# Kernel optimization log

Hardware: AMD Instinct MI355X
Metric: run time of the kernel (lower is better)

The kernel has to match this reference:

```python
import jax, jax.numpy as jnp
import numpy as np
import math

N_NODES = 100000
N_EDGES = 3200000
F_IN = 512
HID = 128
N_CLS = 16


def setup_inputs() -> dict:
    key = jax.random.key(0)
    k = jax.random.split(key, 6)
    x = jax.random.normal(k[0], (N_NODES, F_IN), dtype=jnp.float32)
    edge_index = jax.random.randint(k[1], (2, N_EDGES), 0, N_NODES, dtype=jnp.int32)
    W1 = jax.random.normal(k[2], (F_IN, HID), dtype=jnp.float32) / np.sqrt(F_IN)
    W2 = jax.random.normal(k[3], (HID, HID), dtype=jnp.float32) / np.sqrt(HID)
    W3 = jax.random.normal(k[4], (N_CLS, HID), dtype=jnp.float32) / np.sqrt(HID)
    b3 = jnp.zeros((N_CLS,), dtype=jnp.float32)
    return {"x": x, "edge_index": edge_index, "W1": W1, "W2": W2, "W3": W3, "b3": b3}


def _sym_norm(edge_index, num_nodes, dtype):
    # add self loops with fill_value = trunc(log2(average_node_degree))
    E = edge_index.shape[1]
    fill = float(math.trunc(math.log2(E / num_nodes)))
    loops = jnp.arange(num_nodes, dtype=edge_index.dtype)
    row = jnp.concatenate([edge_index[0], loops])
    col = jnp.concatenate([edge_index[1], loops])
    w = jnp.concatenate([jnp.ones((E,), dtype), jnp.full((num_nodes,), fill, dtype)])
    deg = jax.ops.segment_sum(w, row, num_segments=num_nodes)
    deg_inv_sqrt = jnp.where(deg > 0, jax.lax.rsqrt(deg), 0.0)
    norm = deg_inv_sqrt[row] * w * deg_inv_sqrt[col]
    return row, col, norm


def reference(x, edge_index, W1, W2, W3, b3):
    N = x.shape[0]
    row, col, norm = _sym_norm(edge_index, N, x.dtype)

    def gcn(h, W):
        h = h @ W                                   # [N, d_out]
        msg = norm[:, None] * h[col]                # gather + scale, [E', d_out]
        return jax.ops.segment_sum(msg, row, num_segments=N)

    h = jax.nn.relu(gcn(x, W1))      # layer 1 + srelu (threshold clamped at 0)
    h = gcn(h, W2)                   # layer 2
    # dropout p=0.5 is identity in eval mode
    return h @ W3.T + b3             # linear classifier [N, n_classes]
```

## Files before the change

kernel.cpp:

```cpp
#include <hip/hip_runtime.h>
#include <cmath>

typedef __attribute__((ext_vector_type(8))) short short8;
typedef __attribute__((ext_vector_type(8))) unsigned short ushort8;
typedef __attribute__((ext_vector_type(4))) float f32x4;
typedef __attribute__((ext_vector_type(2))) float f32x2;
typedef __attribute__((ext_vector_type(4))) unsigned int uint4v;
typedef __attribute__((ext_vector_type(2))) int int2v;

#define EPB 4096
#define BCAP 20480

__device__ inline float bf16_lo(unsigned int p) {
  union { unsigned int i; float f; } v; v.i = p << 16; return v.f;
}
__device__ inline float bf16_hi(unsigned int p) {
  union { unsigned int i; float f; } v; v.i = p & 0xffff0000u; return v.f;
}
__device__ inline f32x2 bf2(unsigned int p) {
  union { unsigned int i; float f; } lo, hi;
  lo.i = p << 16;
  hi.i = p & 0xffff0000u;
  return (f32x2){lo.f, hi.f};
}
__device__ inline float bf16u(unsigned short w) {
  union { unsigned int i; float f; } v; v.i = (unsigned int)w << 16; return v.f;
}
__device__ inline unsigned short f32_to_bf16(float f) {
  union { float f; unsigned int i; } v; v.f = f;
  unsigned int x = v.i;
  x += 0x7fffu + ((x >> 16) & 1u);
  return (unsigned short)(x >> 16);
}
__device__ inline unsigned int cvt_pk_bf16(float a, float b) {
  unsigned int r;
  asm("v_cvt_pk_bf16_f32 %0, %1, %2" : "=v"(r) : "v"(a), "v"(b));
  return r;
}
__device__ inline f32x2 pk_add(f32x2 a, f32x2 b) {
  f32x2 d;
  asm("v_pk_add_f32 %0, %1, %2" : "=v"(d) : "v"(a), "v"(b));
  return d;
}

__global__ __launch_bounds__(256) void bin_k(const int* __restrict__ rows,
                                             const int* __restrict__ cols,
                                             int* __restrict__ bucket_cursor,
                                             unsigned int* __restrict__ binned, int E) {
  __shared__ int lhist[256];
  __shared__ int gbase[256];
  __shared__ int loff[256];
  const int t = threadIdx.x;
  const int base = blockIdx.x * EPB;
  lhist[t] = 0;
  __syncthreads();

  int bk[16];
  unsigned int pk[16];
#pragma unroll
  for (int j = 0; j < 16; ++j) {
    int e = base + j * 256 + t;
    if (e < E) {
      int r = rows[e];
      int c = cols[e];
      bk[j] = r >> 9;
      pk[j] = ((unsigned int)(r & 511) << 17) | (unsigned int)c;
      atomicAdd(&lhist[bk[j]], 1);
    } else {
      bk[j] = -1;
    }
  }
  __syncthreads();
  if (lhist[t] > 0) gbase[t] = atomicAdd(&bucket_cursor[t], lhist[t]);
  loff[t] = 0;
  __syncthreads();
#pragma unroll
  for (int j = 0; j < 16; ++j) {
    if (bk[j] >= 0) {
      int rank = gbase[bk[j]] + atomicAdd(&loff[bk[j]], 1);
      if (rank < BCAP) binned[(size_t)bk[j] * BCAP + rank] = pk[j];
    }
  }
}

__global__ __launch_bounds__(1024) void sort_k(const unsigned int* __restrict__ binned,
                                               const int* __restrict__ bucket_cursor,
                                               int2v* __restrict__ rowse,
                                               float* __restrict__ dis,
                                               int* __restrict__ col_sorted,
                                               int* __restrict__ perm,
                                               int N, float fill) {
  __shared__ int sorted[BCAP];
  __shared__ int cnt[512];
  __shared__ int cur[512];
  __shared__ int dh[512];
  __shared__ int wsum[8];
  const int b = blockIdx.x;
  const int t = threadIdx.x;
  const int start = b * BCAP;
  const int rbase = b << 9;
  int c = bucket_cursor[b];
  if (c > BCAP) c = BCAP;

  auto scan512 = [&](int v) -> int {
    int x = v;
#pragma unroll
    for (int d = 1; d < 64; d <<= 1) {
      int u = __shfl_up(x, d, 64);
      if ((t & 63) >= d) x += u;
    }
    if (t < 512 && (t & 63) == 63) wsum[t >> 6] = x;
    __syncthreads();
    if (t < 64) {
      int s = (t < 8) ? wsum[t] : 0;
#pragma unroll
      for (int d = 1; d < 8; d <<= 1) {
        int u = __shfl_up(s, d, 64);
        if (t >= d) s += u;
      }
      if (t < 8) wsum[t] = s;
    }
    __syncthreads();
    int off = (t >= 64 && t < 512) ? wsum[(t >> 6) - 1] : 0;
    return x + off;
  };

  unsigned int ent[20];
#pragma unroll
  for (int j = 0; j < 20; ++j) {
    int i = j * 1024 + t;
    ent[j] = (i < c) ? binned[start + i] : 0xFFFFFFFFu;
  }

  if (t < 512) cnt[t] = 0;
  __syncthreads();
#pragma unroll
  for (int j = 0; j < 20; ++j)
    if (ent[j] != 0xFFFFFFFFu) atomicAdd(&cnt[ent[j] >> 17], 1);
  __syncthreads();

  int v = (t < 512) ? cnt[t] : 0;
  int incl = scan512(v);
  int excl = incl - v;
  if (t < 512) {
    cur[t] = excl;
    int r = rbase + t;
    if (r < N) {
      rowse[r] = (int2v){start + excl, start + excl + v};
      float d = (float)v + fill;
      dis[r] = d > 0.f ? rsqrtf(d) : 0.f;
    }
  }
  __syncthreads();

#pragma unroll
  for (int j = 0; j < 20; ++j) {
    if (ent[j] != 0xFFFFFFFFu) {
      int rl = (int)(ent[j] >> 17);
      int pos = atomicAdd(&cur[rl], 1);
      sorted[pos] = (int)(ent[j] & 0x1FFFFu);
    }
  }
  __syncthreads();

  for (int i = t; i < c; i += 1024)
    col_sorted[start + i] = sorted[i];

  if (t < 512) dh[t] = 0;
  __syncthreads();
  int key = 0;
  if (t < 512) {
    key = 511 - (v < 511 ? v : 511);
    atomicAdd(&dh[key], 1);
  }
  __syncthreads();
  int hv = (t < 512) ? dh[t] : 0;
  int hincl = scan512(hv);
  if (t < 512) dh[t] = hincl - hv;
  __syncthreads();
  if (t < 512) {
    int rank = atomicAdd(&dh[key], 1);
    perm[rbase + rank] = rbase + t;
  }
}

__global__ __launch_bounds__(256) void cast_w_k(const float* __restrict__ W1,
                                                const float* __restrict__ W2,
                                                const float* __restrict__ W3,
                                                unsigned short* __restrict__ W1t,
                                                unsigned short* __restrict__ W2t,
                                                unsigned short* __restrict__ W3b,
                                                int FIN) {
  int g = blockIdx.x * 256 + threadIdx.x;
  int n1 = FIN * 128;
  if (g < n1) {
    int n = g & 127, k = g >> 7;
    W1t[n * FIN + k] = f32_to_bf16(W1[(size_t)k * 128 + n]);
  } else if (g < n1 + 128 * 128) {
    int gg = g - n1;
    int n = gg & 127, k = gg >> 7;
    W2t[n * 128 + k] = f32_to_bf16(W2[k * 128 + n]);
  } else if (g < n1 + 128 * 128 + 16 * 128) {
    int gg = g - n1 - 128 * 128;
    W3b[gg] = f32_to_bf16(W3[gg]);
  }
}

__global__ __launch_bounds__(256) void gemm_k(const void* __restrict__ Aq, int a_is_f32,
                                              int M, int K,
                                              const unsigned short* __restrict__ Bt,
                                              const float* __restrict__ dis,
                                              unsigned short* __restrict__ C) {
  __shared__ unsigned short Al[128 * 40];
  __shared__ unsigned short Bl[128 * 40];
  const int t = threadIdx.x;
  const int bm = blockIdx.x * 128;
  const int lane = t & 63;
  const int wave = t >> 6;
  const int wm = (wave >> 1) * 64;
  const int wn = (wave & 1) * 64;
  const int l15 = lane & 15;
  const int l4 = lane >> 4;

  f32x4 acc[4][4];
#pragma unroll
  for (int a = 0; a < 4; ++a)
#pragma unroll
    for (int b = 0; b < 4; ++b) acc[a][b] = (f32x4){0.f, 0.f, 0.f, 0.f};

  const int am = t >> 1;
  const int ak = (t & 1) * 16;
  const int bn = t >> 1;
  const int bk = (t & 1) * 16;
  const int arow = bm + am;
  const bool arow_ok = arow < M;

  auto load_a = [&](int k0, ushort8& o0, ushort8& o1) {
    o0 = (ushort8){0, 0, 0, 0, 0, 0, 0, 0};
    o1 = (ushort8){0, 0, 0, 0, 0, 0, 0, 0};
    if (arow_ok) {
      if (a_is_f32) {
        const float* p = (const float*)Aq + (size_t)arow * K + k0 + ak;
        f32x4 f0 = *(const f32x4*)(p);
        f32x4 f1 = *(const f32x4*)(p + 4);
        f32x4 f2 = *(const f32x4*)(p + 8);
        f32x4 f3 = *(const f32x4*)(p + 12);
        union { unsigned int u[4]; ushort8 v8; } c0, c1;
        c0.u[0] = cvt_pk_bf16(f0[0], f0[1]);
        c0.u[1] = cvt_pk_bf16(f0[2], f0[3]);
        c0.u[2] = cvt_pk_bf16(f1[0], f1[1]);
        c0.u[3] = cvt_pk_bf16(f1[2], f1[3]);
        c1.u[0] = cvt_pk_bf16(f2[0], f2[1]);
        c1.u[1] = cvt_pk_bf16(f2[2], f2[3]);
        c1.u[2] = cvt_pk_bf16(f3[0], f3[1]);
        c1.u[3] = cvt_pk_bf16(f3[2], f3[3]);
        o0 = c0.v8;
        o1 = c1.v8;
      } else {
        const unsigned short* p = (const unsigned short*)Aq + (size_t)arow * K + k0 + ak;
        o0 = *(const ushort8*)p;
        o1 = *(const ushort8*)(p + 8);
      }
    }
  };

  ushort8 av0, av1;
  load_a(0, av0, av1);
  ushort8 bv0 = *(const ushort8*)(Bt + (size_t)bn * K + bk);
  ushort8 bv1 = *(const ushort8*)(Bt + (size_t)bn * K + bk + 8);

  for (int k0 = 0; k0 < K; k0 += 32) {
    *(ushort8*)&Al[am * 40 + ak] = av0;
    *(ushort8*)&Al[am * 40 + ak + 8] = av1;
    *(ushort8*)&Bl[bn * 40 + bk] = bv0;
    *(ushort8*)&Bl[bn * 40 + bk + 8] = bv1;
    __syncthreads();

    const int kn = k0 + 32;
    if (kn < K) {
      load_a(kn, av0, av1);
      bv0 = *(const ushort8*)(Bt + (size_t)bn * K + kn + bk);
      bv1 = *(const ushort8*)(Bt + (size_t)bn * K + kn + bk + 8);
    }

    short8 af[4];
#pragma unroll
    for (int mt = 0; mt < 4; ++mt)
      af[mt] = *(const short8*)&Al[(wm + mt * 16 + l15) * 40 + l4 * 8];
#pragma unroll
    for (int nt = 0; nt < 4; ++nt) {
      short8 bfr = *(const short8*)&Bl[(wn + nt * 16 + l15) * 40 + l4 * 8];
#pragma unroll
      for (int mt = 0; mt < 4; ++mt)
        acc[mt][nt] = __builtin_amdgcn_mfma_f32_16x16x32_bf16(af[mt], bfr, acc[mt][nt], 0, 0, 0);
    }
    __syncthreads();
  }

#pragma unroll
  for (int mt = 0; mt < 4; ++mt) {
    int rbase = bm + wm + mt * 16 + l4 * 4;
#pragma unroll
    for (int r = 0; r < 4; ++r) {
      int row = rbase + r;
      if (row < M) {
        float dr = dis[row];
#pragma unroll
        for (int nt = 0; nt < 4; ++nt) {
          int col = wn + nt * 16 + l15;
          C[(size_t)row * 128 + col] = f32_to_bf16(acc[mt][nt][r] * dr);
        }
      }
    }
  }
}

__global__ __launch_bounds__(256) void agg_k(const unsigned short* __restrict__ hs,
                                             const int2v* __restrict__ rowse,
                                             const int* __restrict__ cols,
                                             const float* __restrict__ dis,
                                             const int* __restrict__ perm,
                                             unsigned short* __restrict__ out_bf,
                                             const unsigned short* __restrict__ W3b,
                                             const float* __restrict__ b3,
                                             float* __restrict__ fcout,
                                             int N, float fill, int mode) {
  const int q = blockIdx.x * 16 + (threadIdx.x >> 4);
  const unsigned int fl = threadIdx.x & 15;
  const int rid = perm[q];
  if (rid >= N) return;
  const char* __restrict__ hsc = (const char*)hs;
  const unsigned int flo = fl << 4;

  int2v se = rowse[rid];
  int e = se.x;
  const int end = se.y;

  f32x2 a0 = {0.f, 0.f}, a1 = {0.f, 0.f}, a2 = {0.f, 0.f}, a3 = {0.f, 0.f};

  for (; e + 8 <= end; e += 8) {
    unsigned int c0 = (unsigned int)cols[e];
    unsigned int c1 = (unsigned int)cols[e + 1];
    unsigned int c2 = (unsigned int)cols[e + 2];
    unsigned int c3 = (unsigned int)cols[e + 3];
    unsigned int c4 = (unsigned int)cols[e + 4];
    unsigned int c5 = (unsigned int)cols[e + 5];
    unsigned int c6 = (unsigned int)cols[e + 6];
    unsigned int c7 = (unsigned int)cols[e + 7];
    uint4v p0 = *(const uint4v*)(hsc + ((c0 << 8) | flo));
    uint4v p1 = *(const uint4v*)(hsc + ((c1 << 8) | flo));
    uint4v p2 = *(const uint4v*)(hsc + ((c2 << 8) | flo));
    uint4v p3 = *(const uint4v*)(hsc + ((c3 << 8) | flo));
    uint4v p4 = *(const uint4v*)(hsc + ((c4 << 8) | flo));
    uint4v p5 = *(const uint4v*)(hsc + ((c5 << 8) | flo));
    uint4v p6 = *(const uint4v*)(hsc + ((c6 << 8) | flo));
    uint4v p7 = *(const uint4v*)(hsc + ((c7 << 8) | flo));
    a0 = pk_add(a0, bf2(p0[0])); a1 = pk_add(a1, bf2(p0[1]));
    a2 = pk_add(a2, bf2(p0[2])); a3 = pk_add(a3, bf2(p0[3]));
    a0 = pk_add(a0, bf2(p1[0])); a1 = pk_add(a1, bf2(p1[1]));
    a2 = pk_add(a2, bf2(p1[2])); a3 = pk_add(a3, bf2(p1[3]));
    a0 = pk_add(a0, bf2(p2[0])); a1 = pk_add(a1, bf2(p2[1]));
    a2 = pk_add(a2, bf2(p2[2])); a3 = pk_add(a3, bf2(p2[3]));
    a0 = pk_add(a0, bf2(p3[0])); a1 = pk_add(a1, bf2(p3[1]));
    a2 = pk_add(a2, bf2(p3[2])); a3 = pk_add(a3, bf2(p3[3]));
    a0 = pk_add(a0, bf2(p4[0])); a1 = pk_add(a1, bf2(p4[1]));
    a2 = pk_add(a2, bf2(p4[2])); a3 = pk_add(a3, bf2(p4[3]));
    a0 = pk_add(a0, bf2(p5[0])); a1 = pk_add(a1, bf2(p5[1]));
    a2 = pk_add(a2, bf2(p5[2])); a3 = pk_add(a3, bf2(p5[3]));
    a0 = pk_add(a0, bf2(p6[0])); a1 = pk_add(a1, bf2(p6[1]));
    a2 = pk_add(a2, bf2(p6[2])); a3 = pk_add(a3, bf2(p6[3]));
    a0 = pk_add(a0, bf2(p7[0])); a1 = pk_add(a1, bf2(p7[1]));
    a2 = pk_add(a2, bf2(p7[2])); a3 = pk_add(a3, bf2(p7[3]));
  }
  for (; e + 4 <= end; e += 4) {
    unsigned int c0 = (unsigned int)cols[e];
    unsigned int c1 = (unsigned int)cols[e + 1];
    unsigned int c2 = (unsigned int)cols[e + 2];
    unsigned int c3 = (unsigned int)cols[e + 3];
    uint4v p0 = *(const uint4v*)(hsc + ((c0 << 8) | flo));
    uint4v p1 = *(const uint4v*)(hsc + ((c1 << 8) | flo));
    uint4v p2 = *(const uint4v*)(hsc + ((c2 << 8) | flo));
    uint4v p3 = *(const uint4v*)(hsc + ((c3 << 8) | flo));
    a0 = pk_add(a0, bf2(p0[0])); a1 = pk_add(a1, bf2(p0[1]));
    a2 = pk_add(a2, bf2(p0[2])); a3 = pk_add(a3, bf2(p0[3]));
    a0 = pk_add(a0, bf2(p1[0])); a1 = pk_add(a1, bf2(p1[1]));
    a2 = pk_add(a2, bf2(p1[2])); a3 = pk_add(a3, bf2(p1[3]));
    a0 = pk_add(a0, bf2(p2[0])); a1 = pk_add(a1, bf2(p2[1]));
    a2 = pk_add(a2, bf2(p2[2])); a3 = pk_add(a3, bf2(p2[3]));
    a0 = pk_add(a0, bf2(p3[0])); a1 = pk_add(a1, bf2(p3[1]));
    a2 = pk_add(a2, bf2(p3[2])); a3 = pk_add(a3, bf2(p3[3]));
  }
  for (; e < end; ++e) {
    unsigned int c = (unsigned int)cols[e];
    uint4v p = *(const uint4v*)(hsc + ((c << 8) | flo));
    a0 = pk_add(a0, bf2(p[0])); a1 = pk_add(a1, bf2(p[1]));
    a2 = pk_add(a2, bf2(p[2])); a3 = pk_add(a3, bf2(p[3]));
  }

  uint4v ps = *(const uint4v*)(hsc + (((unsigned int)rid << 8) | flo));
  float dr = dis[rid];
  float v[8];
  v[0] = dr * (a0.x + fill * bf16_lo(ps[0]));
  v[1] = dr * (a0.y + fill * bf16_hi(ps[0]));
  v[2] = dr * (a1.x + fill * bf16_lo(ps[1]));
  v[3] = dr * (a1.y + fill * bf16_hi(ps[1]));
  v[4] = dr * (a2.x + fill * bf16_lo(ps[2]));
  v[5] = dr * (a2.y + fill * bf16_hi(ps[2]));
  v[6] = dr * (a3.x + fill * bf16_lo(ps[3]));
  v[7] = dr * (a3.y + fill * bf16_hi(ps[3]));

  if (mode == 0) {
    uint4v o;
#pragma unroll
    for (int k = 0; k < 4; ++k) {
      float f0 = fmaxf(v[2 * k], 0.f);
      float f1 = fmaxf(v[2 * k + 1], 0.f);
      o[k] = cvt_pk_bf16(f0, f1);
    }
    *(uint4v*)((char*)out_bf + (((unsigned int)rid << 8) | flo)) = o;
  } else {
    float p[16];
#pragma unroll
    for (int c = 0; c < 16; ++c) {
      ushort8 wr = *(const ushort8*)(W3b + c * 128 + fl * 8);
      float s = v[0] * bf16u(wr[0]);
      s = fmaf(v[1], bf16u(wr[1]), s);
      s = fmaf(v[2], bf16u(wr[2]), s);
      s = fmaf(v[3], bf16u(wr[3]), s);
      s = fmaf(v[4], bf16u(wr[4]), s);
      s = fmaf(v[5], bf16u(wr[5]), s);
      s = fmaf(v[6], bf16u(wr[6]), s);
      s = fmaf(v[7], bf16u(wr[7]), s);
      p[c] = s;
    }
#pragma unroll
    for (int m = 1; m <= 8; m <<= 1)
#pragma unroll
      for (int c = 0; c < 16; ++c) p[c] += __shfl_xor(p[c], m);
    fcout[(size_t)rid * 16 + fl] = p[fl] + b3[fl];
  }
}

extern "C" void kernel_launch(void* const* d_in, const int* in_sizes, int n_in,
                              void* d_out, int out_size, void* d_ws, size_t ws_size,
                              hipStream_t stream) {
  const float* x  = (const float*)d_in[0];
  const int* edge = (const int*)d_in[1];
  const float* W1 = (const float*)d_in[2];
  const float* W2 = (const float*)d_in[3];
  const float* W3 = (const float*)d_in[4];
  const float* b3 = (const float*)d_in[5];
  float* out = (float*)d_out;

  const int HID = 128;
  const int FIN = in_sizes[2] / HID;
  const int N   = in_sizes[0] / FIN;
  const int E   = in_sizes[1] / 2;
  const float fill = truncf(log2f((float)E / (float)N));

  char* w = (char*)d_ws;
  size_t off = 0;
  auto alloc = [&](size_t bytes) -> void* {
    void* p = w + off;
    off += (bytes + 255) & ~(size_t)255;
    return p;
  };
  const int NB = (N + 511) >> 9;
  float* dis      = (float*)alloc((size_t)N * 4);
  int2v* rowse    = (int2v*)alloc((size_t)N * 8);
  int* perm       = (int*)alloc((size_t)NB * 512 * 4);
  int* col_sorted = (int*)alloc((size_t)NB * BCAP * 4);
  int* bucket_cursor = (int*)alloc(256 * 4);
  unsigned int* binned = (unsigned int*)alloc((size_t)NB * BCAP * 4);
  unsigned short* W1t  = (unsigned short*)alloc((size_t)FIN * 128 * 2);
  unsigned short* W2t  = (unsigned short*)alloc(128 * 128 * 2);
  unsigned short* W3b  = (unsigned short*)alloc(16 * 128 * 2);
  unsigned short* bufA = (unsigned short*)alloc((size_t)N * 128 * 2);
  unsigned short* bufB = (unsigned short*)alloc((size_t)N * 128 * 2);

  const int* rows  = edge;
  const int* colsp = edge + E;

  hipMemsetAsync(bucket_cursor, 0, 256 * 4, stream);
  bin_k<<<(E + EPB - 1) / EPB, 256, 0, stream>>>(rows, colsp, bucket_cursor, binned, E);
  sort_k<<<NB, 1024, 0, stream>>>(binned, bucket_cursor, rowse, dis,
                                  col_sorted, perm, N, fill);
  const int castN = FIN * 128 + 128 * 128 + 16 * 128;
  cast_w_k<<<(castN + 255) / 256, 256, 0, stream>>>(W1, W2, W3, W1t, W2t, W3b, FIN);

  const int gm = (N + 127) / 128;
  gemm_k<<<gm, 256, 0, stream>>>(x, 1, N, FIN, W1t, dis, bufA);
  agg_k<<<NB * 32, 256, 0, stream>>>(bufA, rowse, col_sorted, dis, perm, bufB,
                                     W3b, b3, out, N, fill, 0);
  gemm_k<<<gm, 256, 0, stream>>>(bufB, 0, N, HID, W2t, dis, bufA);
  agg_k<<<NB * 32, 256, 0, stream>>>(bufA, rowse, col_sorted, dis, perm, bufB,
                                     W3b, b3, out, N, fill, 1);
}
```

Before: 639.4 us.

## Fold W2 into classifier weights and drop second GEMM

Precomputes the fused product W2·W3ᵀ (128x16) in the weight-cast kernel and uses it in the final aggregation's classifier. This removes the second 128x128 GEMM launch over all nodes. The second aggregation now reads the layer-1 output directly, which is prescaled by the source degree factor in the first aggregation. Rounding the fused weights to bf16 and skipping the bf16 intermediate of the second GEMM changes numerics slightly. The second aggregation also reads bufB while being handed bufB as its output buffer, though mode 1 does not write it.

```diff
diff --git a/kernel.cpp b/kernel.cpp
--- a/kernel.cpp
+++ b/kernel.cpp
@@ -188,21 +188,22 @@
                                                 const float* __restrict__ W2,
                                                 const float* __restrict__ W3,
                                                 unsigned short* __restrict__ W1t,
-                                                unsigned short* __restrict__ W2t,
-                                                unsigned short* __restrict__ W3b,
+                                                unsigned short* __restrict__ Wfb,
                                                 int FIN) {
   int g = blockIdx.x * 256 + threadIdx.x;
   int n1 = FIN * 128;
   if (g < n1) {
     int n = g & 127, k = g >> 7;
     W1t[n * FIN + k] = f32_to_bf16(W1[(size_t)k * 128 + n]);
-  } else if (g < n1 + 128 * 128) {
+  } else if (g < n1 + 16 * 128) {
     int gg = g - n1;
-    int n = gg & 127, k = gg >> 7;
-    W2t[n * 128 + k] = f32_to_bf16(W2[k * 128 + n]);
-  } else if (g < n1 + 128 * 128 + 16 * 128) {
-    int gg = g - n1 - 128 * 128;
-    W3b[gg] = f32_to_bf16(W3[gg]);
+    int cls = gg >> 7, i = gg & 127;
+    const float* w2r = W2 + (size_t)i * 128;
+    const float* w3r = W3 + (size_t)cls * 128;
+    float s = 0.f;
+#pragma unroll 8
+    for (int o = 0; o < 128; ++o) s = fmaf(w2r[o], w3r[o], s);
+    Wfb[gg] = f32_to_bf16(s);
   }
 }
 
@@ -321,7 +322,7 @@
                                              const float* __restrict__ dis,
                                              const int* __restrict__ perm,
                                              unsigned short* __restrict__ out_bf,
-                                             const unsigned short* __restrict__ W3b,
+                                             const unsigned short* __restrict__ Wfb,
                                              const float* __restrict__ b3,
                                              float* __restrict__ fcout,
                                              int N, float fill, int mode) {
@@ -413,8 +414,8 @@
     uint4v o;
 #pragma unroll
     for (int k = 0; k < 4; ++k) {
-      float f0 = fmaxf(v[2 * k], 0.f);
-      float f1 = fmaxf(v[2 * k + 1], 0.f);
+      float f0 = dr * fmaxf(v[2 * k], 0.f);
+      float f1 = dr * fmaxf(v[2 * k + 1], 0.f);
       o[k] = cvt_pk_bf16(f0, f1);
     }
     *(uint4v*)((char*)out_bf + (((unsigned int)rid << 8) | flo)) = o;
@@ -422,7 +423,7 @@
     float p[16];
 #pragma unroll
     for (int c = 0; c < 16; ++c) {
-      ushort8 wr = *(const ushort8*)(W3b + c * 128 + fl * 8);
+      ushort8 wr = *(const ushort8*)(Wfb + c * 128 + fl * 8);
       float s = v[0] * bf16u(wr[0]);
       s = fmaf(v[1], bf16u(wr[1]), s);
       s = fmaf(v[2], bf16u(wr[2]), s);
@@ -473,8 +474,7 @@
   int* bucket_cursor = (int*)alloc(256 * 4);
   unsigned int* binned = (unsigned int*)alloc((size_t)NB * BCAP * 4);
   unsigned short* W1t  = (unsigned short*)alloc((size_t)FIN * 128 * 2);
-  unsigned short* W2t  = (unsigned short*)alloc(128 * 128 * 2);
-  unsigned short* W3b  = (unsigned short*)alloc(16 * 128 * 2);
+  unsigned short* Wfb  = (unsigned short*)alloc(16 * 128 * 2);
   unsigned short* bufA = (unsigned short*)alloc((size_t)N * 128 * 2);
   unsigned short* bufB = (unsigned short*)alloc((size_t)N * 128 * 2);
 
@@ -485,14 +485,13 @@
   bin_k<<<(E + EPB - 1) / EPB, 256, 0, stream>>>(rows, colsp, bucket_cursor, binned, E);
   sort_k<<<NB, 1024, 0, stream>>>(binned, bucket_cursor, rowse, dis,
                                   col_sorted, perm, N, fill);
-  const int castN = FIN * 128 + 128 * 128 + 16 * 128;
-  cast_w_k<<<(castN + 255) / 256, 256, 0, stream>>>(W1, W2, W3, W1t, W2t, W3b, FIN);
+  const int castN = FIN * 128 + 16 * 128;
+  cast_w_k<<<(castN + 255) / 256, 256, 0, stream>>>(W1, W2, W3, W1t, Wfb, FIN);
 
   const int gm = (N + 127) / 128;
   gemm_k<<<gm, 256, 0, stream>>>(x, 1, N, FIN, W1t, dis, bufA);
   agg_k<<<NB * 32, 256, 0, stream>>>(bufA, rowse, col_sorted, dis, perm, bufB,
-                                     W3b, b3, out, N, fill, 0);
-  gemm_k<<<gm, 256, 0, stream>>>(bufB, 0, N, HID, W2t, dis, bufA);
-  agg_k<<<NB * 32, 256, 0, stream>>>(bufA, rowse, col_sorted, dis, perm, bufB,
-                                     W3b, b3, out, N, fill, 1);
-}
+                                     Wfb, b3, out, N, fill, 0);
+  agg_k<<<NB * 32, 256, 0, stream>>>(bufB, rowse, col_sorted, dis, perm, bufB,
+                                     Wfb, b3, out, N, fill, 1);
+}
```

New measurement: 621.4 us. 2.8% less time.
